# Performance work log

Measured on AMD Instinct MI355X. Metric: run time of the kernel, lower is better.

The kernel has to match this reference:

```python
import jax, jax.numpy as jnp
import numpy as np

VOCAB = 65535
EMB = 1024
CTX = 1024
B = 32
HID = 4 * EMB


def setup_inputs() -> dict:
    key = jax.random.key(0)
    ks = jax.random.split(key, 20)
    s = 0.02
    inp = {
        "idx": jax.random.randint(ks[0], (B, 1), 0, VOCAB),
        "key_cache": jax.random.normal(ks[1], (B, CTX - 1, EMB), jnp.float32),
        "value_cache": jax.random.normal(ks[2], (B, CTX - 1, EMB), jnp.float32),
        "emb_table": jax.random.normal(ks[3], (VOCAB, EMB), jnp.float32) * s,
        "pos_table": jax.random.normal(ks[4], (CTX, EMB), jnp.float32) * s,
        "Wk": jax.random.normal(ks[5], (EMB, EMB), jnp.float32) * s,
        "bk": jnp.zeros((EMB,), jnp.float32),
        "Wv": jax.random.normal(ks[6], (EMB, EMB), jnp.float32) * s,
        "bv": jnp.zeros((EMB,), jnp.float32),
        "Wq": jax.random.normal(ks[7], (EMB, EMB), jnp.float32) * s,
        "bq": jnp.zeros((EMB,), jnp.float32),
        "W1": jax.random.normal(ks[8], (EMB, HID), jnp.float32) * s,
        "b1": jnp.zeros((HID,), jnp.float32),
        "W2": jax.random.normal(ks[9], (HID, EMB), jnp.float32) * s,
        "b2": jnp.zeros((EMB,), jnp.float32),
        "Wl": jax.random.normal(ks[10], (EMB, VOCAB), jnp.float32) * s,
        "bl": jnp.zeros((VOCAB,), jnp.float32),
    }
    return inp


def reference(idx, key_cache, value_cache, emb_table, pos_table,
              Wk, bk, Wv, bv, Wq, bq, W1, b1, W2, b2, Wl, bl):
    # token + position embeddings (seq_len=1, positions = arange(1) = [0])
    tok = emb_table[idx]                      # [B, 1, D]
    pos = pos_table[:1][None, :, :]           # [1, 1, D]
    x = tok + pos                             # [B, 1, D]

    # cache truncation to last context_size-1 steps (no-op here at 1023)
    kc = key_cache[:, -(CTX - 1):, :]
    vc = value_cache[:, -(CTX - 1):, :]

    # single-head attention with KV cache
    k_new = x @ Wk + bk                       # [B, 1, D]
    v_new = x @ Wv + bv
    q_new = x @ Wq + bq
    keys = jnp.concatenate([kc, k_new], axis=1)    # [B, S, D]
    values = jnp.concatenate([vc, v_new], axis=1)  # [B, S, D]
    scale = 1.0 / jnp.sqrt(jnp.asarray(EMB, x.dtype))
    scores = jnp.einsum("bqd,bsd->bqs", q_new, keys) * scale  # [B, 1, S]
    probs = jax.nn.softmax(scores, axis=-1)
    attn_out = jnp.einsum("bqs,bsd->bqd", probs, values)      # [B, 1, D]

    # feed-forward (exact GELU, matching torch nn.GELU default)
    h = jax.nn.gelu(attn_out @ W1 + b1, approximate=False)
    ffn_out = h @ W2 + b2                     # [B, 1, D]

    logits = ffn_out @ Wl + bl                # [B, 1, VOCAB]
    return logits
```

## Files before the change

kernel.cpp:

```cpp
#include <hip/hip_runtime.h>
#include <cstddef>

#define BATCH 32
#define EMBD 1024
#define SCTX 1023
#define CTXF 1024
#define HIDD 4096
#define VOC 65535

__global__ void embed_kernel(const int* __restrict__ idx, const float* __restrict__ emb,
                             const float* __restrict__ pos, float* __restrict__ x) {
  int b = blockIdx.x, t = threadIdx.x;
  const float4* er = (const float4*)(emb + (size_t)idx[b] * EMBD);
  const float4* pr = (const float4*)pos;
  float4 e = er[t], p = pr[t];
  ((float4*)(x + (size_t)b * EMBD))[t] = make_float4(e.x + p.x, e.y + p.y, e.z + p.z, e.w + p.w);
}

template <int CHK>
__global__ __launch_bounds__(256) void skgemm_lds(const float* __restrict__ X,
                                                  const float* __restrict__ W,
                                                  float* __restrict__ Pout, int N, int K) {
  __shared__ float xt[CHK][BATCH];
  int t = threadIdx.x;
  int p = blockIdx.y;
  int i0 = p * CHK;
  for (int m = t; m < CHK * BATCH; m += 256) {
    int i = m >> 5, b = m & 31;
    xt[i][b] = X[b * K + i0 + i];
  }
  __syncthreads();

  int j = blockIdx.x * 256 + t;
  float acc[BATCH];
#pragma unroll
  for (int b = 0; b < BATCH; ++b) acc[b] = 0.f;
  const float* wp = W + (size_t)i0 * N + j;
#pragma unroll 8
  for (int i = 0; i < CHK; ++i) {
    float w = wp[(size_t)i * N];
#pragma unroll
    for (int b = 0; b < BATCH; ++b) acc[b] = fmaf(xt[i][b], w, acc[b]);
  }
#pragma unroll
  for (int b = 0; b < BATCH; ++b) Pout[((size_t)p * BATCH + b) * N + j] = acc[b];
}

template <int CHK>
__global__ __launch_bounds__(256) void qkv_lds(const float* __restrict__ X,
                                               const float* __restrict__ Wk,
                                               const float* __restrict__ Wv,
                                               const float* __restrict__ Wq,
                                               float* __restrict__ Pout, int nch) {
  __shared__ float xt[CHK][BATCH];
  int t = threadIdx.x;
  int p = blockIdx.y;
  int i0 = p * CHK;
  for (int m = t; m < CHK * BATCH; m += 256) {
    int i = m >> 5, b = m & 31;
    xt[i][b] = X[b * EMBD + i0 + i];
  }
  __syncthreads();

  const float* __restrict__ W = (blockIdx.z == 0) ? Wk : (blockIdx.z == 1) ? Wv : Wq;
  int j = blockIdx.x * 256 + t;
  float acc[BATCH];
#pragma unroll
  for (int b = 0; b < BATCH; ++b) acc[b] = 0.f;
  const float* wp = W + (size_t)i0 * EMBD + j;
#pragma unroll 8
  for (int i = 0; i < CHK; ++i) {
    float w = wp[(size_t)i * EMBD];
#pragma unroll
    for (int b = 0; b < BATCH; ++b) acc[b] = fmaf(xt[i][b], w, acc[b]);
  }
#pragma unroll
  for (int b = 0; b < BATCH; ++b)
    Pout[((size_t)(blockIdx.z * nch + p) * BATCH + b) * EMBD + j] = acc[b];
}

__global__ void reduce_qkv(const float* __restrict__ part, int P,
                           const float* __restrict__ bk, const float* __restrict__ bv,
                           const float* __restrict__ bq,
                           float* __restrict__ kout, float* __restrict__ vout,
                           float* __restrict__ qout) {
  int z = blockIdx.y;
  int m = blockIdx.x * 256 + threadIdx.x;
  float s = 0.f;
  for (int p = 0; p < P; ++p) s += part[(size_t)(z * P + p) * (BATCH * EMBD) + m];
  const float* bias = (z == 0) ? bk : (z == 1) ? bv : bq;
  float* out = (z == 0) ? kout : (z == 1) ? vout : qout;
  out[m] = s + bias[m & (EMBD - 1)];
}

__global__ void reduce_ep(const float* __restrict__ part, int P,
                          const float* __restrict__ bias, float* __restrict__ out,
                          int total, int mask, int act) {
  int m = blockIdx.x * 256 + threadIdx.x;
  if (m >= total) return;
  float s = 0.f;
  for (int p = 0; p < P; ++p) s += part[(size_t)p * total + m];
  if (bias) s += bias[m & mask];
  if (act == 1) s = 0.5f * s * (1.f + erff(s * 0.70710678118654752f));
  out[m] = s;
}

__global__ void reduce_ffn2(const float* __restrict__ part, int P,
                            const float* __restrict__ bias, float* __restrict__ out,
                            float* __restrict__ out_t) {
  int m = blockIdx.x * 256 + threadIdx.x;
  float s = 0.f;
  for (int p = 0; p < P; ++p) s += part[(size_t)p * (BATCH * EMBD) + m];
  s += bias[m & (EMBD - 1)];
  out[m] = s;
  out_t[(size_t)(m & (EMBD - 1)) * BATCH + (m >> 10)] = s;
}

__global__ void scores_kernel(const float* __restrict__ q, const float* __restrict__ kcache,
                              const float* __restrict__ knew, float* __restrict__ scores) {
  int b = blockIdx.y;
  int wave = threadIdx.x >> 6, lane = threadIdx.x & 63;
  const float* qb = q + (size_t)b * EMBD;
  float4 qf[4];
#pragma unroll
  for (int r = 0; r < 4; ++r) qf[r] = *(const float4*)(qb + r * 256 + lane * 4);
  int sbase = blockIdx.x * 16 + wave * 4;
  const float* kr[4];
  float acc[4] = {0.f, 0.f, 0.f, 0.f};
#pragma unroll
  for (int it = 0; it < 4; ++it) {
    int s = sbase + it;
    kr[it] = (s < SCTX) ? (kcache + ((size_t)b * SCTX + s) * EMBD)
                        : (knew + (size_t)b * EMBD);
  }
#pragma unroll
  for (int r = 0; r < 4; ++r) {
#pragma unroll
    for (int it = 0; it < 4; ++it) {
      float4 kf = *(const float4*)(kr[it] + r * 256 + lane * 4);
      acc[it] += qf[r].x * kf.x + qf[r].y * kf.y + qf[r].z * kf.z + qf[r].w * kf.w;
    }
  }
#pragma unroll
  for (int it = 0; it < 4; ++it) {
    float a = acc[it];
#pragma unroll
    for (int m = 32; m > 0; m >>= 1) a += __shfl_xor(a, m, 64);
    if (lane == 0) scores[(size_t)b * CTXF + sbase + it] = a * 0.03125f;
  }
}

__global__ void softmax_kernel(float* __restrict__ sc) {
  int b = blockIdx.x;
  int t = threadIdx.x;
  __shared__ float red[16];
  float v = sc[(size_t)b * CTXF + t];
  float m = v;
#pragma unroll
  for (int d = 32; d > 0; d >>= 1) m = fmaxf(m, __shfl_xor(m, d, 64));
  if ((t & 63) == 0) red[t >> 6] = m;
  __syncthreads();
  float bm = red[0];
#pragma unroll
  for (int w = 1; w < 16; ++w) bm = fmaxf(bm, red[w]);
  float e = expf(v - bm);
  __syncthreads();
  float s = e;
#pragma unroll
  for (int d = 32; d > 0; d >>= 1) s += __shfl_xor(s, d, 64);
  if ((t & 63) == 0) red[t >> 6] = s;
  __syncthreads();
  float bs = 0.f;
#pragma unroll
  for (int w = 0; w < 16; ++w) bs += red[w];
  sc[(size_t)b * CTXF + t] = e / bs;
}

__global__ void pv_kernel(const float* __restrict__ probs, const float* __restrict__ vcache,
                          const float* __restrict__ vnew, float* __restrict__ part) {
  int b = blockIdx.y;
  int p = blockIdx.x;
  int t = threadIdx.x;
  float acc[4] = {0.f, 0.f, 0.f, 0.f};
  int s0 = p * 32;
#pragma unroll 4
  for (int s = s0; s < s0 + 32; ++s) {
    float pr = probs[(size_t)b * CTXF + s];
    const float* vrow = (s < SCTX) ? (vcache + ((size_t)b * SCTX + s) * EMBD)
                                   : (vnew + (size_t)b * EMBD);
#pragma unroll
    for (int r = 0; r < 4; ++r) acc[r] = fmaf(pr, vrow[t + r * 256], acc[r]);
  }
#pragma unroll
  for (int r = 0; r < 4; ++r) part[((size_t)p * BATCH + b) * EMBD + t + r * 256] = acc[r];
}

__global__ __launch_bounds__(256) void logits_v5(const float* __restrict__ Xt,
                                                 const float* __restrict__ Wl,
                                                 float* __restrict__ part) {
  int t = threadIdx.x;
  int p = blockIdx.y;
  int q0 = p * 256;

  int jb = blockIdx.x * 512;
  int j0 = jb + t;
  int j1 = jb + 256 + t;
  bool v1 = (j1 < VOC);
  float acc0[BATCH], acc1[BATCH];
#pragma unroll
  for (int b = 0; b < BATCH; ++b) { acc0[b] = 0.f; acc1[b] = 0.f; }

  const float* wp = Wl + (size_t)q0 * VOC;
  const float* xp = Xt + (size_t)q0 * BATCH;
#pragma unroll 4
  for (int i = 0; i < 256; ++i) {
    float w0 = wp[(size_t)i * VOC + j0];
    float w1 = v1 ? wp[(size_t)i * VOC + j1] : 0.f;
    const float* xr = xp + i * BATCH;
#pragma unroll
    for (int b4 = 0; b4 < 8; ++b4) {
      float4 xv = *(const float4*)(xr + b4 * 4);
      acc0[b4 * 4 + 0] = fmaf(xv.x, w0, acc0[b4 * 4 + 0]);
      acc0[b4 * 4 + 1] = fmaf(xv.y, w0, acc0[b4 * 4 + 1]);
      acc0[b4 * 4 + 2] = fmaf(xv.z, w0, acc0[b4 * 4 + 2]);
      acc0[b4 * 4 + 3] = fmaf(xv.w, w0, acc0[b4 * 4 + 3]);
      acc1[b4 * 4 + 0] = fmaf(xv.x, w1, acc1[b4 * 4 + 0]);
      acc1[b4 * 4 + 1] = fmaf(xv.y, w1, acc1[b4 * 4 + 1]);
      acc1[b4 * 4 + 2] = fmaf(xv.z, w1, acc1[b4 * 4 + 2]);
      acc1[b4 * 4 + 3] = fmaf(xv.w, w1, acc1[b4 * 4 + 3]);
    }
  }
#pragma unroll
  for (int b = 0; b < BATCH; ++b) {
    float* pr = part + ((size_t)p * BATCH + b) * VOC;
    pr[j0] = acc0[b];
    if (v1) pr[j1] = acc1[b];
  }
}

__global__ void logits_reduce(const float* __restrict__ part, const float* __restrict__ bl,
                              float* __restrict__ out) {
  size_t m = (size_t)blockIdx.x * 256 + threadIdx.x;
  if (m >= (size_t)BATCH * VOC) return;
  int j = (int)(m % VOC);
  float s = 0.f;
#pragma unroll
  for (int p = 0; p < 4; ++p) s += part[(size_t)p * BATCH * VOC + m];
  out[m] = s + bl[j];
}

__global__ void logits_splitb(const float* __restrict__ X, const float* __restrict__ Wl,
                              const float* __restrict__ bl, float* __restrict__ out) {
  int j = blockIdx.x * 256 + threadIdx.x;
  if (j >= VOC) return;
  int b0 = blockIdx.y * 16;
  float acc[16];
#pragma unroll
  for (int b = 0; b < 16; ++b) acc[b] = 0.f;
#pragma unroll 8
  for (int i = 0; i < EMBD; ++i) {
    float w = Wl[(size_t)i * VOC + j];
#pragma unroll
    for (int b = 0; b < 16; ++b) acc[b] = fmaf(X[(b0 + b) * EMBD + i], w, acc[b]);
  }
  float bb = bl[j];
#pragma unroll
  for (int b = 0; b < 16; ++b) out[(size_t)(b0 + b) * VOC + j] = acc[b] + bb;
}

extern "C" void kernel_launch(void* const* d_in, const int* in_sizes, int n_in,
                              void* d_out, int out_size, void* d_ws, size_t ws_size,
                              hipStream_t stream) {
  const int* idx = (const int*)d_in[0];
  const float* key_cache = (const float*)d_in[1];
  const float* value_cache = (const float*)d_in[2];
  const float* emb_table = (const float*)d_in[3];
  const float* pos_table = (const float*)d_in[4];
  const float* Wk = (const float*)d_in[5];
  const float* bk = (const float*)d_in[6];
  const float* Wv = (const float*)d_in[7];
  const float* bv = (const float*)d_in[8];
  const float* Wq = (const float*)d_in[9];
  const float* bq = (const float*)d_in[10];
  const float* W1 = (const float*)d_in[11];
  const float* b1 = (const float*)d_in[12];
  const float* W2 = (const float*)d_in[13];
  const float* b2 = (const float*)d_in[14];
  const float* Wl = (const float*)d_in[15];
  const float* bl = (const float*)d_in[16];
  float* out = (float*)d_out;

  float* ws = (float*)d_ws;
  float* x    = ws;
  float* k    = ws + 32768;
  float* v    = ws + 65536;
  float* q    = ws + 98304;
  float* prob = ws + 131072;
  float* attn = ws + 163840;
  float* h    = ws + 196608;
  float* ffn  = ws + 327680;
  float* xt_g = ws + 360448;
  float* part = ws + 393216;

  size_t partCap = (ws_size / 4 > 393216) ? ws_size / 4 - 393216 : 0;

  embed_kernel<<<dim3(BATCH), 256, 0, stream>>>(idx, emb_table, pos_table, x);

  if (partCap >= (size_t)3 * 32 * BATCH * EMBD) {
    qkv_lds<32><<<dim3(4, 32, 3), 256, 0, stream>>>(x, Wk, Wv, Wq, part, 32);
    reduce_qkv<<<dim3(128, 3), 256, 0, stream>>>(part, 32, bk, bv, bq, k, v, q);
  } else {
    qkv_lds<128><<<dim3(4, 8, 3), 256, 0, stream>>>(x, Wk, Wv, Wq, part, 8);
    reduce_qkv<<<dim3(128, 3), 256, 0, stream>>>(part, 8, bk, bv, bq, k, v, q);
  }

  scores_kernel<<<dim3(64, BATCH), 256, 0, stream>>>(q, key_cache, k, prob);
  softmax_kernel<<<dim3(BATCH), 1024, 0, stream>>>(prob);
  pv_kernel<<<dim3(32, BATCH), 256, 0, stream>>>(prob, value_cache, v, part);
  reduce_ep<<<dim3(128), 256, 0, stream>>>(part, 32, nullptr, attn, BATCH * EMBD, 0, 0);

  skgemm_lds<64><<<dim3(16, 16), 256, 0, stream>>>(attn, W1, part, HIDD, EMBD);
  reduce_ep<<<dim3(512), 256, 0, stream>>>(part, 16, b1, h, BATCH * HIDD, HIDD - 1, 1);

  skgemm_lds<64><<<dim3(4, 64), 256, 0, stream>>>(h, W2, part, EMBD, HIDD);
  reduce_ffn2<<<dim3(128), 256, 0, stream>>>(part, 64, b2, ffn, xt_g);

  if (partCap >= (size_t)4 * BATCH * VOC) {
    logits_v5<<<dim3(128, 4), 256, 0, stream>>>(xt_g, Wl, part);
    logits_reduce<<<dim3(8192), 256, 0, stream>>>(part, bl, out);
  } else {
    logits_splitb<<<dim3(256, 2), 256, 0, stream>>>(ffn, Wl, bl, out);
  }
}
```

Before: 245.9 us.

## Drop split-K logits with separate reduce; compute full K per column with fused bias

The logits GEMV no longer splits K into four partials with a separate reduction kernel. Each thread now handles one vocab column over all 1024 inputs and adds the bias directly into the output. This removes the write and re-read of a large partial-sum buffer and one kernel launch. In exchange the grid drops to 256 blocks with one column per thread, which lowers parallelism and the memory-level parallelism available to hide latency on the Wl stream.

After: 446.5 us. 1.82x slower.

```diff
diff --git a/kernel.cpp b/kernel.cpp
--- a/kernel.cpp
+++ b/kernel.cpp
@@ -195,77 +195,34 @@
   for (int r = 0; r < 4; ++r) part[((size_t)p * BATCH + b) * EMBD + t + r * 256] = acc[r];
 }
 
-__global__ __launch_bounds__(256) void logits_v5(const float* __restrict__ Xt,
+__global__ __launch_bounds__(256) void logits_v6(const float* __restrict__ Xt,
                                                  const float* __restrict__ Wl,
-                                                 float* __restrict__ part) {
-  int t = threadIdx.x;
-  int p = blockIdx.y;
-  int q0 = p * 256;
-
-  int jb = blockIdx.x * 512;
-  int j0 = jb + t;
-  int j1 = jb + 256 + t;
-  bool v1 = (j1 < VOC);
-  float acc0[BATCH], acc1[BATCH];
-#pragma unroll
-  for (int b = 0; b < BATCH; ++b) { acc0[b] = 0.f; acc1[b] = 0.f; }
-
-  const float* wp = Wl + (size_t)q0 * VOC;
-  const float* xp = Xt + (size_t)q0 * BATCH;
-#pragma unroll 4
-  for (int i = 0; i < 256; ++i) {
-    float w0 = wp[(size_t)i * VOC + j0];
-    float w1 = v1 ? wp[(size_t)i * VOC + j1] : 0.f;
-    const float* xr = xp + i * BATCH;
+                                                 const float* __restrict__ bl,
+                                                 float* __restrict__ out) {
+  int j = blockIdx.x * 256 + threadIdx.x;
+  bool jv = (j < VOC);
+  int jc = jv ? j : (VOC - 1);
+  float acc[BATCH];
+#pragma unroll
+  for (int b = 0; b < BATCH; ++b) acc[b] = 0.f;
+
+#pragma unroll 16
+  for (int i = 0; i < EMBD; ++i) {
+    float w = Wl[(size_t)i * VOC + jc];
+    const float* xr = Xt + i * BATCH;
 #pragma unroll
     for (int b4 = 0; b4 < 8; ++b4) {
       float4 xv = *(const float4*)(xr + b4 * 4);
-      acc0[b4 * 4 + 0] = fmaf(xv.x, w0, acc0[b4 * 4 + 0]);
-      acc0[b4 * 4 + 1] = fmaf(xv.y, w0, acc0[b4 * 4 + 1]);
-      acc0[b4 * 4 + 2] = fmaf(xv.z, w0, acc0[b4 * 4 + 2]);
-      acc0[b4 * 4 + 3] = fmaf(xv.w, w0, acc0[b4 * 4 + 3]);
-      acc1[b4 * 4 + 0] = fmaf(xv.x, w1, acc1[b4 * 4 + 0]);
-      acc1[b4 * 4 + 1] = fmaf(xv.y, w1, acc1[b4 * 4 + 1]);
-      acc1[b4 * 4 + 2] = fmaf(xv.z, w1, acc1[b4 * 4 + 2]);
-      acc1[b4 * 4 + 3] = fmaf(xv.w, w1, acc1[b4 * 4 + 3]);
+      acc[b4 * 4 + 0] = fmaf(xv.x, w, acc[b4 * 4 + 0]);
+      acc[b4 * 4 + 1] = fmaf(xv.y, w, acc[b4 * 4 + 1]);
+      acc[b4 * 4 + 2] = fmaf(xv.z, w, acc[b4 * 4 + 2]);
+      acc[b4 * 4 + 3] = fmaf(xv.w, w, acc[b4 * 4 + 3]);
     }
   }
-#pragma unroll
-  for (int b = 0; b < BATCH; ++b) {
-    float* pr = part + ((size_t)p * BATCH + b) * VOC;
-    pr[j0] = acc0[b];
-    if (v1) pr[j1] = acc1[b];
-  }
-}
-
-__global__ void logits_reduce(const float* __restrict__ part, const float* __restrict__ bl,
-                              float* __restrict__ out) {
-  size_t m = (size_t)blockIdx.x * 256 + threadIdx.x;
-  if (m >= (size_t)BATCH * VOC) return;
-  int j = (int)(m % VOC);
-  float s = 0.f;
-#pragma unroll
-  for (int p = 0; p < 4; ++p) s += part[(size_t)p * BATCH * VOC + m];
-  out[m] = s + bl[j];
-}
-
-__global__ void logits_splitb(const float* __restrict__ X, const float* __restrict__ Wl,
-                              const float* __restrict__ bl, float* __restrict__ out) {
-  int j = blockIdx.x * 256 + threadIdx.x;
-  if (j >= VOC) return;
-  int b0 = blockIdx.y * 16;
-  float acc[16];
-#pragma unroll
-  for (int b = 0; b < 16; ++b) acc[b] = 0.f;
-#pragma unroll 8
-  for (int i = 0; i < EMBD; ++i) {
-    float w = Wl[(size_t)i * VOC + j];
-#pragma unroll
-    for (int b = 0; b < 16; ++b) acc[b] = fmaf(X[(b0 + b) * EMBD + i], w, acc[b]);
-  }
+  if (!jv) return;
   float bb = bl[j];
 #pragma unroll
-  for (int b = 0; b < 16; ++b) out[(size_t)(b0 + b) * VOC + j] = acc[b] + bb;
+  for (int b = 0; b < BATCH; ++b) out[(size_t)b * VOC + j] = acc[b] + bb;
 }
 
 extern "C" void kernel_launch(void* const* d_in, const int* in_sizes, int n_in,
@@ -325,10 +282,5 @@
   skgemm_lds<64><<<dim3(4, 64), 256, 0, stream>>>(h, W2, part, EMBD, HIDD);
   reduce_ffn2<<<dim3(128), 256, 0, stream>>>(part, 64, b2, ffn, xt_g);
 
-  if (partCap >= (size_t)4 * BATCH * VOC) {
-    logits_v5<<<dim3(128, 4), 256, 0, stream>>>(xt_g, Wl, part);
-    logits_reduce<<<dim3(8192), 256, 0, stream>>>(part, bl, out);
-  } else {
-    logits_splitb<<<dim3(256, 2), 256, 0, stream>>>(ffn, Wl, bl, out);
-  }
-}
+  logits_v6<<<dim3(256), 256, 0, stream>>>(xt_g, Wl, bl, out);
+}
```
